# Kernel tuning notes

Measured on AMD Instinct MI355X. Metric: run time of the kernel, lower is better.

Reference implementation:

```python
import jax, jax.numpy as jnp
import numpy as np

N_LAYERS = 2
D_MODEL = 1024
D_INNER = 2 * D_MODEL
D_STATE = 16
D_CONV = 4
DT_RANK = D_MODEL // 16  # 64
B_SZ, L = 1, 2048
EPS = 1e-5


def layernorm(x, w, b):
    mu = jnp.mean(x, axis=-1, keepdims=True)
    var = jnp.mean(jnp.square(x - mu), axis=-1, keepdims=True)
    return (x - mu) * jax.lax.rsqrt(var + EPS) * w + b


def mamba(x, in_w, cw, cb, xp_w, dtp_w, dtp_b, A_log, Dp, out_w):
    # x: [B, L, D_MODEL]
    Bn, Ln, _ = x.shape
    xz = jnp.einsum('bld,ed->ble', x, in_w)          # [B,L,2*D_INNER]
    xc, z = jnp.split(xz, 2, axis=-1)
    # causal depthwise conv1d (kernel D_CONV)
    xp = jnp.pad(xc, ((0, 0), (D_CONV - 1, 0), (0, 0)))
    xc = sum(xp[:, k:k + Ln, :] * cw[:, k] for k in range(D_CONV)) + cb
    xc = jax.nn.silu(xc)
    dbl = jnp.einsum('ble,re->blr', xc, xp_w)        # [B,L,DT_RANK+2*D_STATE]
    dt, Bm, Cm = jnp.split(dbl, [DT_RANK, DT_RANK + D_STATE], axis=-1)
    dt = jax.nn.softplus(jnp.einsum('blr,er->ble', dt, dtp_w) + dtp_b)  # [B,L,E]
    A = -jnp.exp(A_log)                              # [E,N], strictly negative
    dA = jnp.exp(dt[..., None] * A)                  # [B,L,E,N]
    dBu = (dt * xc)[..., None] * Bm[:, :, None, :]   # [B,L,E,N]

    def step(h, inp):
        dA_t, dBu_t, C_t = inp
        h = dA_t * h + dBu_t                         # [B,E,N]
        y = jnp.einsum('ben,bn->be', h, C_t)
        return h, y

    h0 = jnp.zeros((Bn, D_INNER, D_STATE), dA.dtype)
    _, ys = jax.lax.scan(step, h0, (dA.transpose(1, 0, 2, 3),
                                    dBu.transpose(1, 0, 2, 3),
                                    Cm.transpose(1, 0, 2)))
    y = ys.transpose(1, 0, 2) + xc * Dp              # [B,L,E]
    y = y * jax.nn.silu(z)
    return jnp.einsum('ble,de->bld', y, out_w)       # [B,L,D_MODEL]


def setup_inputs() -> dict:
    key = jax.random.key(0)
    ks = jax.random.split(key, 12)
    s = 0.02
    dt_init = np.log(np.expm1(0.01)).astype(np.float32)  # softplus^-1(0.01)
    A_row = jnp.log(jnp.arange(1, D_STATE + 1, dtype=jnp.float32))
    return {
        'x': jax.random.normal(ks[0], (B_SZ, L, D_MODEL), jnp.float32),
        'ln_w': jnp.ones((N_LAYERS, D_MODEL), jnp.float32),
        'ln_b': jnp.zeros((N_LAYERS, D_MODEL), jnp.float32),
        'in_proj_w': jax.random.normal(ks[1], (N_LAYERS, 2 * D_INNER, D_MODEL)) * s,
        'conv_w': jax.random.normal(ks[2], (N_LAYERS, D_INNER, D_CONV)) * 0.2,
        'conv_b': jnp.zeros((N_LAYERS, D_INNER), jnp.float32),
        'x_proj_w': jax.random.normal(ks[3], (N_LAYERS, DT_RANK + 2 * D_STATE, D_INNER)) * s,
        'dt_proj_w': jax.random.normal(ks[4], (N_LAYERS, D_INNER, DT_RANK)) * (DT_RANK ** -0.5),
        'dt_proj_b': jnp.full((N_LAYERS, D_INNER), dt_init),
        'A_log': jnp.broadcast_to(A_row, (N_LAYERS, D_INNER, D_STATE)).copy(),
        'D_skip': jnp.ones((N_LAYERS, D_INNER), jnp.float32),
        'out_proj_w': jax.random.normal(ks[5], (N_LAYERS, D_MODEL, D_INNER)) * s,
        'norm_f_w': jnp.ones((D_MODEL,), jnp.float32),
        'norm_f_b': jnp.zeros((D_MODEL,), jnp.float32),
    }


def reference(x, ln_w, ln_b, in_proj_w, conv_w, conv_b, x_proj_w, dt_proj_w,
              dt_proj_b, A_log, D_skip, out_proj_w, norm_f_w, norm_f_b):
    for i in range(N_LAYERS):
        h = layernorm(x, ln_w[i], ln_b[i])
        h = mamba(h, in_proj_w[i], conv_w[i], conv_b[i], x_proj_w[i],
                  dt_proj_w[i], dt_proj_b[i], A_log[i], D_skip[i], out_proj_w[i])
        x = h + x  # residual (dropout/drop_path are identity in eval)
    return layernorm(x, norm_f_w, norm_f_b)
```

## Files before the change

### kernel.cpp

```cpp
#include <hip/hip_runtime.h>
#include <hip/hip_bf16.h>
#include <math.h>

#define LSEQ 2048
#define DMODEL 1024
#define DINNER 2048
#define DSTATE 16
#define DCONV 4
#define DTRANK 64
#define RPROJ 96

#define CHUNK 16
#define NCHUNK (LSEQ / CHUNK)

#define XSPLIT 4

typedef __attribute__((ext_vector_type(8))) short bf16x8;
typedef __attribute__((ext_vector_type(4))) float f32x4;

__device__ __forceinline__ float softplusf(float x) {
    return (x > 20.f) ? x : log1pf(__expf(x));
}
__device__ __forceinline__ float siluf(float x) {
    return x / (1.f + __expf(-x));
}
__device__ __forceinline__ short f2bf(float f) {
    union { float f; unsigned u; } v; v.f = f;
    unsigned r = v.u + 0x7FFFu + ((v.u >> 16) & 1u);
    return (short)(r >> 16);
}
__device__ __forceinline__ float bf2f(short h) {
    union { unsigned u; float f; } v;
    v.u = ((unsigned)(unsigned short)h) << 16;
    return v.f;
}

__device__ __forceinline__ void cvt8(const float* __restrict__ s,
                                     short* __restrict__ d, int i) {
    const float4 a = *(const float4*)(s + i);
    const float4 b = *(const float4*)(s + i + 4);
    alignas(16) short h[8];
    h[0] = f2bf(a.x); h[1] = f2bf(a.y); h[2] = f2bf(a.z); h[3] = f2bf(a.w);
    h[4] = f2bf(b.x); h[5] = f2bf(b.y); h[6] = f2bf(b.z); h[7] = f2bf(b.w);
    *(uint4*)(d + i) = *(const uint4*)h;
}

__global__ __launch_bounds__(256) void cvt_weights(
    const float* __restrict__ s0, short* __restrict__ d0, int n0,
    const float* __restrict__ s1, short* __restrict__ d1, int n1,
    const float* __restrict__ s2, short* __restrict__ d2, int n2,
    const float* __restrict__ s3, short* __restrict__ d3, int n3)
{
    int i = (blockIdx.x * 256 + threadIdx.x) * 8;
    if (i < n0) { cvt8(s0, d0, i); return; }
    i -= n0;
    if (i < n1) { cvt8(s1, d1, i); return; }
    i -= n1;
    if (i < n2) { cvt8(s2, d2, i); return; }
    i -= n2;
    if (i < n3) { cvt8(s3, d3, i); return; }
}

__global__ __launch_bounds__(256) void ln_kernel(
    const float* __restrict__ x, const float* __restrict__ w,
    const float* __restrict__ b, float* __restrict__ outf,
    short* __restrict__ outb)
{
    __shared__ float s1[256], s2[256];
    const int row = blockIdx.x;
    const int tid = threadIdx.x;
    const float* xr = x + (size_t)row * DMODEL;
    float v[4];
    float s = 0.f, sq = 0.f;
#pragma unroll
    for (int k = 0; k < 4; k++) {
        v[k] = xr[k * 256 + tid];
        s += v[k];
        sq += v[k] * v[k];
    }
    s1[tid] = s; s2[tid] = sq;
    __syncthreads();
    for (int off = 128; off > 0; off >>= 1) {
        if (tid < off) { s1[tid] += s1[tid + off]; s2[tid] += s2[tid + off]; }
        __syncthreads();
    }
    const float mu = s1[0] * (1.f / DMODEL);
    const float var = s2[0] * (1.f / DMODEL) - mu * mu;
    const float rstd = rsqrtf(var + 1e-5f);
#pragma unroll
    for (int k = 0; k < 4; k++) {
        const int i = k * 256 + tid;
        const float o = (v[k] - mu) * rstd * w[i] + b[i];
        if (outf) outf[(size_t)row * DMODEL + i] = o;
        if (outb) outb[(size_t)row * DMODEL + i] = f2bf(o);
    }
}

template<int MI, int NJ, int MODE>
__global__ __launch_bounds__(256) void gemm_mfma(
    const short* __restrict__ A, int lda,
    const short* __restrict__ W, int ldw,
    float* __restrict__ Cf, short* __restrict__ Cb, int ldc,
    int M, int N, int K,
    const float* __restrict__ resid)
{
    constexpr int BM = 32 * MI;
    constexpr int BN = 32 * NJ;
    constexpr int AISS = BM / 32;
    constexpr int WISS = BN / 32;
    __shared__ alignas(16) short As[BM * 64];
    __shared__ alignas(16) short Ws[BN * 64];

    const int tid = threadIdx.x;
    const int lane = tid & 63;
    const int w = tid >> 6;
    const int wr = w >> 1, wc = w & 1;
    const int row0 = blockIdx.y * BM;
    const int col0 = blockIdx.x * BN;
    const int kbeg = blockIdx.z * K;

    const int srow = tid >> 3;
    const int dch  = tid & 7;
    const int skch = (dch ^ (srow & 7)) * 8;

    f32x4 acc[MI][NJ];
#pragma unroll
    for (int i = 0; i < MI; i++)
#pragma unroll
        for (int j = 0; j < NJ; j++) acc[i][j] = (f32x4)0.f;

    const int lrow = lane & 15;
    const int q = lane >> 4;

    for (int kt = kbeg; kt < kbeg + K; kt += 64) {
        __syncthreads();
#pragma unroll
        for (int j = 0; j < AISS; j++) {
            const short* gp = A + (size_t)(row0 + j * 32 + srow) * lda + kt + skch;
            __builtin_amdgcn_global_load_lds(
                (const __attribute__((address_space(1))) void*)gp,
                (__attribute__((address_space(3))) void*)(&As[j * 2048 + tid * 8]),
                16, 0, 0);
        }
#pragma unroll
        for (int j = 0; j < WISS; j++) {
            const int wrow = col0 + j * 32 + srow;
            if (wrow < N) {
                const short* gp = W + (size_t)wrow * ldw + kt + skch;
                __builtin_amdgcn_global_load_lds(
                    (const __attribute__((address_space(1))) void*)gp,
                    (__attribute__((address_space(3))) void*)(&Ws[j * 2048 + tid * 8]),
                    16, 0, 0);
            }
        }
        __syncthreads();

#pragma unroll
        for (int ks = 0; ks < 2; ks++) {
            bf16x8 af[MI], bfr[NJ];
#pragma unroll
            for (int i = 0; i < MI; i++) {
                const int R = wr * (16 * MI) + i * 16 + lrow;
                const int pc = (ks * 4 + q) ^ (R & 7);
                af[i] = *(const bf16x8*)&As[R * 64 + pc * 8];
            }
#pragma unroll
            for (int j = 0; j < NJ; j++) {
                const int R = wc * (16 * NJ) + j * 16 + lrow;
                const int pc = (ks * 4 + q) ^ (R & 7);
                bfr[j] = *(const bf16x8*)&Ws[R * 64 + pc * 8];
            }
#pragma unroll
            for (int i = 0; i < MI; i++)
#pragma unroll
                for (int j = 0; j < NJ; j++)
                    acc[i][j] = __builtin_amdgcn_mfma_f32_16x16x32_bf16(
                        af[i], bfr[j], acc[i][j], 0, 0, 0);
        }
    }

    const int rbase = row0 + wr * (16 * MI);
    const int cbase = col0 + wc * (16 * NJ);
#pragma unroll
    for (int i = 0; i < MI; i++) {
#pragma unroll
        for (int j = 0; j < NJ; j++) {
            const int gcol = cbase + j * 16 + lrow;
            if (gcol < N) {
#pragma unroll
                for (int r = 0; r < 4; r++) {
                    const int grow = rbase + i * 16 + (lane >> 4) * 4 + r;
                    float v = acc[i][j][r];
                    if (MODE == 2) {
                        Cf[(size_t)grow * ldc + gcol] =
                            v + resid[(size_t)grow * ldc + gcol];
                    } else if (MODE == 3) {
                        Cb[(size_t)grow * ldc + gcol] = f2bf(v);
                    } else {
                        atomicAdd(&Cf[(size_t)grow * ldc + gcol], v);
                    }
                }
            }
        }
    }
}

__global__ __launch_bounds__(256) void dtproj_kernel(
    const float* __restrict__ dbl,
    const short* __restrict__ dtp_w,
    const float* __restrict__ dtp_b,
    short* __restrict__ dt_bf)
{
    __shared__ alignas(16) short As[64 * 32];
    __shared__ alignas(16) short Ws[128 * 32];
    const int tid = threadIdx.x;
    const int lane = tid & 63;
    const int w = tid >> 6;
    const int wr = w >> 1, wc = w & 1;
    const int row0 = blockIdx.y * 64;
    const int col0 = blockIdx.x * 128;
    const int srow = tid >> 2;
    const int skch = ((tid & 3) ^ ((srow >> 1) & 3)) * 8;
    const int lrow = lane & 15;
    const int q = lane >> 4;

    f32x4 acc[2][4];
#pragma unroll
    for (int i = 0; i < 2; i++)
#pragma unroll
        for (int j = 0; j < 4; j++) acc[i][j] = (f32x4)0.f;

#pragma unroll
    for (int kt = 0; kt < 64; kt += 32) {
        __syncthreads();
        {
            const float* gp = dbl + (size_t)(row0 + srow) * RPROJ + kt + skch;
            const float4 a = *(const float4*)gp;
            const float4 b = *(const float4*)(gp + 4);
            alignas(16) short h[8];
            h[0] = f2bf(a.x); h[1] = f2bf(a.y); h[2] = f2bf(a.z); h[3] = f2bf(a.w);
            h[4] = f2bf(b.x); h[5] = f2bf(b.y); h[6] = f2bf(b.z); h[7] = f2bf(b.w);
            *(uint4*)(As + tid * 8) = *(const uint4*)h;
        }
#pragma unroll
        for (int j = 0; j < 2; j++) {
            const short* gp = dtp_w + (size_t)(col0 + j * 64 + srow) * DTRANK + kt + skch;
            __builtin_amdgcn_global_load_lds(
                (const __attribute__((address_space(1))) void*)gp,
                (__attribute__((address_space(3))) void*)(&Ws[j * 2048 + tid * 8]),
                16, 0, 0);
        }
        __syncthreads();

        bf16x8 af[2], bfr[4];
#pragma unroll
        for (int i = 0; i < 2; i++) {
            const int R = wr * 32 + i * 16 + lrow;
            af[i] = *(const bf16x8*)&As[R * 32 + ((q ^ ((R >> 1) & 3)) * 8)];
        }
#pragma unroll
        for (int j = 0; j < 4; j++) {
            const int R = wc * 64 + j * 16 + lrow;
            bfr[j] = *(const bf16x8*)&Ws[R * 32 + ((q ^ ((R >> 1) & 3)) * 8)];
        }
#pragma unroll
        for (int i = 0; i < 2; i++)
#pragma unroll
            for (int j = 0; j < 4; j++)
                acc[i][j] = __builtin_amdgcn_mfma_f32_16x16x32_bf16(
                    af[i], bfr[j], acc[i][j], 0, 0, 0);
    }

    const int rbase = row0 + wr * 32;
    const int cbase = col0 + wc * 64;
#pragma unroll
    for (int i = 0; i < 2; i++)
#pragma unroll
        for (int j = 0; j < 4; j++) {
            const int gcol = cbase + j * 16 + lrow;
#pragma unroll
            for (int r = 0; r < 4; r++) {
                const int grow = rbase + i * 16 + (lane >> 4) * 4 + r;
                dt_bf[(size_t)grow * DINNER + gcol] =
                    f2bf(softplusf(acc[i][j][r] + dtp_b[gcol]));
            }
        }
}

__global__ __launch_bounds__(256) void conv_silu_kernel(
    const short* __restrict__ xzb, const float* __restrict__ cw,
    const float* __restrict__ cb, short* __restrict__ xcb,
    float* __restrict__ dbl_zero)
{
    const int g = blockIdx.x * 256 + threadIdx.x;
    if (g < (LSEQ * RPROJ) / 4)
        *(float4*)(dbl_zero + g * 4) = make_float4(0.f, 0.f, 0.f, 0.f);
    const int t = g >> 8;
    const int c0 = (g & 255) * 8;
    float acc[8];
#pragma unroll
    for (int j = 0; j < 8; j++) acc[j] = cb[c0 + j];
#pragma unroll
    for (int k = 0; k < DCONV; k++) {
        const int tt = t - (DCONV - 1) + k;
        if (tt >= 0) {
            const bf16x8 v = *(const bf16x8*)(xzb + (size_t)tt * (2 * DINNER) + c0);
#pragma unroll
            for (int j = 0; j < 8; j++)
                acc[j] += bf2f(v[j]) * cw[(c0 + j) * DCONV + k];
        }
    }
    alignas(16) short h[8];
#pragma unroll
    for (int j = 0; j < 8; j++) h[j] = f2bf(siluf(acc[j]));
    *(uint4*)(xcb + (size_t)t * DINNER + c0) = *(const uint4*)h;
}

__global__ __launch_bounds__(256) void scan_pass1(
    const short* __restrict__ dtb,
    const short* __restrict__ xcb,
    const float* __restrict__ dbl,
    const float* __restrict__ A_log,
    float* __restrict__ S,
    float* __restrict__ sumdt)
{
    const int e = blockIdx.x * 256 + threadIdx.x;
    const int c = blockIdx.y;
    float a[DSTATE];
#pragma unroll
    for (int n = 0; n < DSTATE; n++) a[n] = -__expf(A_log[(size_t)e * DSTATE + n]);
    float h[DSTATE];
#pragma unroll
    for (int n = 0; n < DSTATE; n++) h[n] = 0.f;
    float sd = 0.f;

    __shared__ float sBC[CHUNK][32];
    for (int i = threadIdx.x; i < CHUNK * 32; i += 256) {
        const int tl = i >> 5, j = i & 31;
        sBC[tl][j] = dbl[(size_t)(c * CHUNK + tl) * RPROJ + DTRANK + j];
    }
    __syncthreads();

    const size_t rb = (size_t)c * CHUNK * DINNER + e;
    short dt_c = dtb[rb], xc_c = xcb[rb];
#pragma unroll
    for (int tl = 0; tl < CHUNK; tl++) {
        short dt_n = 0, xc_n = 0;
        if (tl + 1 < CHUNK) {
            dt_n = dtb[rb + (size_t)(tl + 1) * DINNER];
            xc_n = xcb[rb + (size_t)(tl + 1) * DINNER];
        }
        const float dtv = bf2f(dt_c);
        const float du = dtv * bf2f(xc_c);
        sd += dtv;
#pragma unroll
        for (int n = 0; n < DSTATE; n++) {
            const float dA = __expf(dtv * a[n]);
            h[n] = dA * h[n] + du * sBC[tl][n];
        }
        dt_c = dt_n; xc_c = xc_n;
    }
    sumdt[(size_t)c * DINNER + e] = sd;
#pragma unroll
    for (int n = 0; n < DSTATE; n++)
        S[((size_t)c * DSTATE + n) * DINNER + e] = h[n];
}

__global__ __launch_bounds__(256) void scan_pass2(
    const float* __restrict__ A_log,
    const float* __restrict__ sumdt,
    float* __restrict__ S)
{
    const int idx = blockIdx.x * 256 + threadIdx.x;
    const int e = idx & (DINNER - 1);
    const int n = idx >> 11;
    const float a = -__expf(A_log[(size_t)e * DSTATE + n]);
    const size_t base = (size_t)n * DINNER + e;
    const size_t cstr = (size_t)DSTATE * DINNER;
    float H = 0.f;
    for (int c = 0; c < NCHUNK; c += 4) {
        const float sc0 = S[base + (size_t)(c + 0) * cstr];
        const float sc1 = S[base + (size_t)(c + 1) * cstr];
        const float sc2 = S[base + (size_t)(c + 2) * cstr];
        const float sc3 = S[base + (size_t)(c + 3) * cstr];
        const float sd0 = sumdt[(size_t)(c + 0) * DINNER + e];
        const float sd1 = sumdt[(size_t)(c + 1) * DINNER + e];
        const float sd2 = sumdt[(size_t)(c + 2) * DINNER + e];
        const float sd3 = sumdt[(size_t)(c + 3) * DINNER + e];
        S[base + (size_t)(c + 0) * cstr] = H;
        H = __expf(a * sd0) * H + sc0;
        S[base + (size_t)(c + 1) * cstr] = H;
        H = __expf(a * sd1) * H + sc1;
        S[base + (size_t)(c + 2) * cstr] = H;
        H = __expf(a * sd2) * H + sc2;
        S[base + (size_t)(c + 3) * cstr] = H;
        H = __expf(a * sd3) * H + sc3;
    }
}

__global__ __launch_bounds__(256) void scan_pass3(
    const short* __restrict__ dtb,
    const short* __restrict__ xcb,
    const float* __restrict__ dbl,
    const short* __restrict__ xzb,
    const float* __restrict__ A_log,
    const float* __restrict__ Dp,
    const float* __restrict__ S,
    short* __restrict__ yb)
{
    const int e = blockIdx.x * 256 + threadIdx.x;
    const int c = blockIdx.y;
    float a[DSTATE];
#pragma unroll
    for (int n = 0; n < DSTATE; n++) a[n] = -__expf(A_log[(size_t)e * DSTATE + n]);
    float h[DSTATE];
#pragma unroll
    for (int n = 0; n < DSTATE; n++)
        h[n] = S[((size_t)c * DSTATE + n) * DINNER + e];
    const float dskip = Dp[e];

    __shared__ float sBC[CHUNK][32];
    for (int i = threadIdx.x; i < CHUNK * 32; i += 256) {
        const int tl = i >> 5, j = i & 31;
        sBC[tl][j] = dbl[(size_t)(c * CHUNK + tl) * RPROJ + DTRANK + j];
    }
    __syncthreads();

    const size_t rb = (size_t)c * CHUNK * DINNER + e;
    const size_t zb = (size_t)c * CHUNK * (2 * DINNER) + DINNER + e;
    short dt_c = dtb[rb], xc_c = xcb[rb], z_c = xzb[zb];
#pragma unroll
    for (int tl = 0; tl < CHUNK; tl++) {
        short dt_n = 0, xc_n = 0, z_n = 0;
        if (tl + 1 < CHUNK) {
            dt_n = dtb[rb + (size_t)(tl + 1) * DINNER];
            xc_n = xcb[rb + (size_t)(tl + 1) * DINNER];
            z_n = xzb[zb + (size_t)(tl + 1) * (2 * DINNER)];
        }
        const float dtv = bf2f(dt_c);
        const float xcv = bf2f(xc_c);
        const float du = dtv * xcv;
        float yv = 0.f;
#pragma unroll
        for (int n = 0; n < DSTATE; n++) {
            const float dA = __expf(dtv * a[n]);
            h[n] = dA * h[n] + du * sBC[tl][n];
            yv += h[n] * sBC[tl][16 + n];
        }
        yv = (yv + xcv * dskip) * siluf(bf2f(z_c));
        yb[rb + (size_t)tl * DINNER] = f2bf(yv);
        dt_c = dt_n; xc_c = xc_n; z_c = z_n;
    }
}

extern "C" void kernel_launch(void* const* d_in, const int* in_sizes, int n_in,
                              void* d_out, int out_size, void* d_ws, size_t ws_size,
                              hipStream_t stream) {
    const float* x_in   = (const float*)d_in[0];
    const float* ln_w   = (const float*)d_in[1];
    const float* ln_b   = (const float*)d_in[2];
    const float* in_w   = (const float*)d_in[3];
    const float* conv_w = (const float*)d_in[4];
    const float* conv_b = (const float*)d_in[5];
    const float* xp_w   = (const float*)d_in[6];
    const float* dtp_w  = (const float*)d_in[7];
    const float* dtp_b  = (const float*)d_in[8];
    const float* A_log  = (const float*)d_in[9];
    const float* D_skip = (const float*)d_in[10];
    const float* out_w  = (const float*)d_in[11];
    const float* nf_w   = (const float*)d_in[12];
    const float* nf_b   = (const float*)d_in[13];
    float* out = (float*)d_out;

    float* w = (float*)d_ws;
    float* buf_x = w; w += (size_t)LSEQ * DMODEL;
    float* dbl   = w; w += (size_t)LSEQ * RPROJ;
    float* Sbuf  = w; w += (size_t)NCHUNK * DSTATE * DINNER;
    float* sumdt = w; w += (size_t)NCHUNK * DINNER;
    short* h_bf    = (short*)w; w += (size_t)LSEQ * DMODEL / 2;
    short* xz_bf   = (short*)w; w += (size_t)LSEQ * 2 * DINNER / 2;
    short* xc_bf   = (short*)w; w += (size_t)LSEQ * DINNER / 2;
    short* dt_bf   = (short*)w; w += (size_t)LSEQ * DINNER / 2;
    short* y_bf    = (short*)w; w += (size_t)LSEQ * DINNER / 2;
    short* in_w_bf  = (short*)w; w += (size_t)2 * (2 * DINNER) * DMODEL / 2;
    short* xp_w_bf  = (short*)w; w += (size_t)2 * RPROJ * DINNER / 2;
    short* dtp_w_bf = (short*)w; w += (size_t)2 * DINNER * DTRANK / 2;
    short* out_w_bf = (short*)w; w += (size_t)2 * DMODEL * DINNER / 2;

    {
        const int n1 = 2 * (2 * DINNER) * DMODEL;
        const int n2 = 2 * RPROJ * DINNER;
        const int n3 = 2 * DMODEL * DINNER;
        const int n4 = 2 * DINNER * DTRANK;
        const int total = n1 + n2 + n3 + n4;
        cvt_weights<<<dim3(total / (256 * 8)), dim3(256), 0, stream>>>(
            in_w, in_w_bf, n1, xp_w, xp_w_bf, n2,
            out_w, out_w_bf, n3, dtp_w, dtp_w_bf, n4);
    }

    for (int layer = 0; layer < 2; layer++) {
        const float* resid_src = (layer == 0) ? x_in : buf_x;
        ln_kernel<<<dim3(LSEQ), dim3(256), 0, stream>>>(
            resid_src, ln_w + layer * DMODEL, ln_b + layer * DMODEL,
            nullptr, h_bf);
        gemm_mfma<4, 4, 3><<<dim3((2 * DINNER) / 128, LSEQ / 128), dim3(256), 0, stream>>>(
            h_bf, DMODEL, in_w_bf + (size_t)layer * 2 * DINNER * DMODEL, DMODEL,
            nullptr, xz_bf, 2 * DINNER, LSEQ, 2 * DINNER, DMODEL, nullptr);
        conv_silu_kernel<<<dim3((LSEQ * DINNER / 8) / 256), dim3(256), 0, stream>>>(
            xz_bf, conv_w + (size_t)layer * DINNER * DCONV, conv_b + layer * DINNER,
            xc_bf, dbl);
        gemm_mfma<2, 2, 6><<<dim3(2, LSEQ / 64, XSPLIT), dim3(256), 0, stream>>>(
            xc_bf, DINNER, xp_w_bf + (size_t)layer * RPROJ * DINNER, DINNER,
            dbl, nullptr, RPROJ, LSEQ, RPROJ, DINNER / XSPLIT, nullptr);
        dtproj_kernel<<<dim3(DINNER / 128, LSEQ / 64), dim3(256), 0, stream>>>(
            dbl, dtp_w_bf + (size_t)layer * DINNER * DTRANK,
            dtp_b + layer * DINNER, dt_bf);
        const float* Al = A_log + (size_t)layer * DINNER * DSTATE;
        scan_pass1<<<dim3(DINNER / 256, NCHUNK), dim3(256), 0, stream>>>(
            dt_bf, xc_bf, dbl, Al, Sbuf, sumdt);
        scan_pass2<<<dim3((DINNER * DSTATE) / 256), dim3(256), 0, stream>>>(
            Al, sumdt, Sbuf);
        scan_pass3<<<dim3(DINNER / 256, NCHUNK), dim3(256), 0, stream>>>(
            dt_bf, xc_bf, dbl, xz_bf, Al, D_skip + layer * DINNER, Sbuf, y_bf);
        gemm_mfma<4, 2, 2><<<dim3(DMODEL / 64, LSEQ / 128), dim3(256), 0, stream>>>(
            y_bf, DINNER, out_w_bf + (size_t)layer * DMODEL * DINNER, DINNER,
            buf_x, nullptr, DMODEL, LSEQ, DMODEL, DINNER, resid_src);
    }
    ln_kernel<<<dim3(LSEQ), dim3(256), 0, stream>>>(buf_x, nf_w, nf_b, out, nullptr);
}
```

Measured before the change: 456.9 us.

## Fuse weight conversion with first layernorm, use wave-per-row LN, larger scan chunks

Merges the weight fp32-to-bf16 conversion kernel with the first layer's layernorm into one launch. Rewrites layernorm so each 64-lane wave handles one row with shuffle reductions instead of shared-memory tree reductions. Doubles the scan chunk size to halve the number of chunks carried between passes, and limits scan loop unrolling. This cuts launches and sync overhead, but longer chunks reduce scan parallelism.

```diff
diff --git a/kernel.cpp b/kernel.cpp
--- a/kernel.cpp
+++ b/kernel.cpp
@@ -10,7 +10,7 @@
 #define DTRANK 64
 #define RPROJ 96
 
-#define CHUNK 16
+#define CHUNK 32
 #define NCHUNK (LSEQ / CHUNK)
 
 #define XSPLIT 4
@@ -45,64 +45,81 @@
     *(uint4*)(d + i) = *(const uint4*)h;
 }
 
-__global__ __launch_bounds__(256) void cvt_weights(
-    const float* __restrict__ s0, short* __restrict__ d0, int n0,
-    const float* __restrict__ s1, short* __restrict__ d1, int n1,
-    const float* __restrict__ s2, short* __restrict__ d2, int n2,
-    const float* __restrict__ s3, short* __restrict__ d3, int n3)
-{
-    int i = (blockIdx.x * 256 + threadIdx.x) * 8;
-    if (i < n0) { cvt8(s0, d0, i); return; }
-    i -= n0;
-    if (i < n1) { cvt8(s1, d1, i); return; }
-    i -= n1;
-    if (i < n2) { cvt8(s2, d2, i); return; }
-    i -= n2;
-    if (i < n3) { cvt8(s3, d3, i); return; }
-}
-
-__global__ __launch_bounds__(256) void ln_kernel(
+__device__ __forceinline__ void ln_phase(
+    const float* __restrict__ x, const float* __restrict__ w,
+    const float* __restrict__ b, float* __restrict__ outf,
+    short* __restrict__ outb, int bid, int tid)
+{
+    const int wv = tid >> 6, lane = tid & 63;
+    const int row = bid * 4 + wv;
+    const float* xr = x + (size_t)row * DMODEL;
+    float v[16];
+    float s = 0.f, sq = 0.f;
+#pragma unroll
+    for (int k = 0; k < 16; k++) {
+        v[k] = xr[k * 64 + lane];
+        s += v[k];
+        sq += v[k] * v[k];
+    }
+#pragma unroll
+    for (int off = 32; off > 0; off >>= 1) {
+        s += __shfl_xor(s, off, 64);
+        sq += __shfl_xor(sq, off, 64);
+    }
+    const float mu = s * (1.f / DMODEL);
+    const float var = sq * (1.f / DMODEL) - mu * mu;
+    const float rstd = rsqrtf(var + 1e-5f);
+#pragma unroll
+    for (int k = 0; k < 16; k++) {
+        const int i = k * 64 + lane;
+        const float o = (v[k] - mu) * rstd * w[i] + b[i];
+        if (outf) outf[(size_t)row * DMODEL + i] = o;
+        else      outb[(size_t)row * DMODEL + i] = f2bf(o);
+    }
+}
+
+__global__ __launch_bounds__(256) void cvt_ln_kernel(
+    const float* __restrict__ in_w, short* __restrict__ in_w_bf,
+    const float* __restrict__ xp_w, short* __restrict__ xp_w_bf,
+    const float* __restrict__ out_w, short* __restrict__ out_w_bf,
+    const float* __restrict__ dtp_w, short* __restrict__ dtp_w_bf,
+    const float* __restrict__ x_in, const float* __restrict__ ln_w,
+    const float* __restrict__ ln_b, short* __restrict__ h_bf)
+{
+    const int n1 = 2 * (2 * DINNER) * DMODEL;
+    const int n2 = 2 * RPROJ * DINNER;
+    const int n3 = 2 * DMODEL * DINNER;
+    const int bid = blockIdx.x;
+    const int tid = threadIdx.x;
+    {
+        int i = (bid * 256 + tid) * 8;
+        if (i < n1) { cvt8(in_w, in_w_bf, i); goto done_cvt; }
+        i -= n1;
+        if (i < n2) { cvt8(xp_w, xp_w_bf, i); goto done_cvt; }
+        i -= n2;
+        if (i < n3) { cvt8(out_w, out_w_bf, i); goto done_cvt; }
+        i -= n3;
+        cvt8(dtp_w, dtp_w_bf, i);
+    }
+done_cvt:
+    if (bid < LSEQ / 4)
+        ln_phase(x_in, ln_w, ln_b, nullptr, h_bf, bid, tid);
+}
+
+__global__ __launch_bounds__(256) void ln_g(
     const float* __restrict__ x, const float* __restrict__ w,
     const float* __restrict__ b, float* __restrict__ outf,
     short* __restrict__ outb)
 {
-    __shared__ float s1[256], s2[256];
-    const int row = blockIdx.x;
-    const int tid = threadIdx.x;
-    const float* xr = x + (size_t)row * DMODEL;
-    float v[4];
-    float s = 0.f, sq = 0.f;
-#pragma unroll
-    for (int k = 0; k < 4; k++) {
-        v[k] = xr[k * 256 + tid];
-        s += v[k];
-        sq += v[k] * v[k];
-    }
-    s1[tid] = s; s2[tid] = sq;
-    __syncthreads();
-    for (int off = 128; off > 0; off >>= 1) {
-        if (tid < off) { s1[tid] += s1[tid + off]; s2[tid] += s2[tid + off]; }
-        __syncthreads();
-    }
-    const float mu = s1[0] * (1.f / DMODEL);
-    const float var = s2[0] * (1.f / DMODEL) - mu * mu;
-    const float rstd = rsqrtf(var + 1e-5f);
-#pragma unroll
-    for (int k = 0; k < 4; k++) {
-        const int i = k * 256 + tid;
-        const float o = (v[k] - mu) * rstd * w[i] + b[i];
-        if (outf) outf[(size_t)row * DMODEL + i] = o;
-        if (outb) outb[(size_t)row * DMODEL + i] = f2bf(o);
-    }
+    ln_phase(x, w, b, outf, outb, blockIdx.x, threadIdx.x);
 }
 
 template<int MI, int NJ, int MODE>
-__global__ __launch_bounds__(256) void gemm_mfma(
+__global__ __launch_bounds__(256) void gemm_g(
     const short* __restrict__ A, int lda,
     const short* __restrict__ W, int ldw,
     float* __restrict__ Cf, short* __restrict__ Cb, int ldc,
-    int M, int N, int K,
-    const float* __restrict__ resid)
+    int N, int K, const float* __restrict__ resid)
 {
     constexpr int BM = 32 * MI;
     constexpr int BN = 32 * NJ;
@@ -205,7 +222,7 @@
     }
 }
 
-__global__ __launch_bounds__(256) void dtproj_kernel(
+__global__ __launch_bounds__(256) void dtproj_g(
     const float* __restrict__ dbl,
     const short* __restrict__ dtp_w,
     const float* __restrict__ dtp_b,
@@ -287,7 +304,7 @@
         }
 }
 
-__global__ __launch_bounds__(256) void conv_silu_kernel(
+__global__ __launch_bounds__(256) void conv_g(
     const short* __restrict__ xzb, const float* __restrict__ cw,
     const float* __restrict__ cb, short* __restrict__ xcb,
     float* __restrict__ dbl_zero)
@@ -316,7 +333,7 @@
     *(uint4*)(xcb + (size_t)t * DINNER + c0) = *(const uint4*)h;
 }
 
-__global__ __launch_bounds__(256) void scan_pass1(
+__global__ __launch_bounds__(256) void scan1_g(
     const short* __restrict__ dtb,
     const short* __restrict__ xcb,
     const float* __restrict__ dbl,
@@ -343,7 +360,7 @@
 
     const size_t rb = (size_t)c * CHUNK * DINNER + e;
     short dt_c = dtb[rb], xc_c = xcb[rb];
-#pragma unroll
+#pragma unroll 4
     for (int tl = 0; tl < CHUNK; tl++) {
         short dt_n = 0, xc_n = 0;
         if (tl + 1 < CHUNK) {
@@ -366,7 +383,7 @@
         S[((size_t)c * DSTATE + n) * DINNER + e] = h[n];
 }
 
-__global__ __launch_bounds__(256) void scan_pass2(
+__global__ __launch_bounds__(256) void scan2_g(
     const float* __restrict__ A_log,
     const float* __restrict__ sumdt,
     float* __restrict__ S)
@@ -398,7 +415,7 @@
     }
 }
 
-__global__ __launch_bounds__(256) void scan_pass3(
+__global__ __launch_bounds__(256) void scan3_g(
     const short* __restrict__ dtb,
     const short* __restrict__ xcb,
     const float* __restrict__ dbl,
@@ -429,7 +446,7 @@
     const size_t rb = (size_t)c * CHUNK * DINNER + e;
     const size_t zb = (size_t)c * CHUNK * (2 * DINNER) + DINNER + e;
     short dt_c = dtb[rb], xc_c = xcb[rb], z_c = xzb[zb];
-#pragma unroll
+#pragma unroll 4
     for (int tl = 0; tl < CHUNK; tl++) {
         short dt_n = 0, xc_n = 0, z_n = 0;
         if (tl + 1 < CHUNK) {
@@ -488,43 +505,41 @@
     short* out_w_bf = (short*)w; w += (size_t)2 * DMODEL * DINNER / 2;
 
     {
-        const int n1 = 2 * (2 * DINNER) * DMODEL;
-        const int n2 = 2 * RPROJ * DINNER;
-        const int n3 = 2 * DMODEL * DINNER;
-        const int n4 = 2 * DINNER * DTRANK;
-        const int total = n1 + n2 + n3 + n4;
-        cvt_weights<<<dim3(total / (256 * 8)), dim3(256), 0, stream>>>(
-            in_w, in_w_bf, n1, xp_w, xp_w_bf, n2,
-            out_w, out_w_bf, n3, dtp_w, dtp_w_bf, n4);
+        const int total = 2 * (2 * DINNER) * DMODEL + 2 * RPROJ * DINNER
+                        + 2 * DMODEL * DINNER + 2 * DINNER * DTRANK;
+        cvt_ln_kernel<<<dim3(total / (256 * 8)), dim3(256), 0, stream>>>(
+            in_w, in_w_bf, xp_w, xp_w_bf, out_w, out_w_bf, dtp_w, dtp_w_bf,
+            x_in, ln_w, ln_b, h_bf);
     }
 
     for (int layer = 0; layer < 2; layer++) {
         const float* resid_src = (layer == 0) ? x_in : buf_x;
-        ln_kernel<<<dim3(LSEQ), dim3(256), 0, stream>>>(
-            resid_src, ln_w + layer * DMODEL, ln_b + layer * DMODEL,
-            nullptr, h_bf);
-        gemm_mfma<4, 4, 3><<<dim3((2 * DINNER) / 128, LSEQ / 128), dim3(256), 0, stream>>>(
+        if (layer > 0)
+            ln_g<<<dim3(LSEQ / 4), dim3(256), 0, stream>>>(
+                resid_src, ln_w + layer * DMODEL, ln_b + layer * DMODEL,
+                nullptr, h_bf);
+        gemm_g<4, 4, 3><<<dim3((2 * DINNER) / 128, LSEQ / 128), dim3(256), 0, stream>>>(
             h_bf, DMODEL, in_w_bf + (size_t)layer * 2 * DINNER * DMODEL, DMODEL,
-            nullptr, xz_bf, 2 * DINNER, LSEQ, 2 * DINNER, DMODEL, nullptr);
-        conv_silu_kernel<<<dim3((LSEQ * DINNER / 8) / 256), dim3(256), 0, stream>>>(
+            nullptr, xz_bf, 2 * DINNER, 2 * DINNER, DMODEL, nullptr);
+        conv_g<<<dim3((LSEQ * DINNER / 8) / 256), dim3(256), 0, stream>>>(
             xz_bf, conv_w + (size_t)layer * DINNER * DCONV, conv_b + layer * DINNER,
             xc_bf, dbl);
-        gemm_mfma<2, 2, 6><<<dim3(2, LSEQ / 64, XSPLIT), dim3(256), 0, stream>>>(
+        gemm_g<2, 2, 6><<<dim3(2, LSEQ / 64, XSPLIT), dim3(256), 0, stream>>>(
             xc_bf, DINNER, xp_w_bf + (size_t)layer * RPROJ * DINNER, DINNER,
-            dbl, nullptr, RPROJ, LSEQ, RPROJ, DINNER / XSPLIT, nullptr);
-        dtproj_kernel<<<dim3(DINNER / 128, LSEQ / 64), dim3(256), 0, stream>>>(
+            dbl, nullptr, RPROJ, RPROJ, DINNER / XSPLIT, nullptr);
+        dtproj_g<<<dim3(DINNER / 128, LSEQ / 64), dim3(256), 0, stream>>>(
             dbl, dtp_w_bf + (size_t)layer * DINNER * DTRANK,
             dtp_b + layer * DINNER, dt_bf);
         const float* Al = A_log + (size_t)layer * DINNER * DSTATE;
-        scan_pass1<<<dim3(DINNER / 256, NCHUNK), dim3(256), 0, stream>>>(
+        scan1_g<<<dim3(DINNER / 256, NCHUNK), dim3(256), 0, stream>>>(
             dt_bf, xc_bf, dbl, Al, Sbuf, sumdt);
-        scan_pass2<<<dim3((DINNER * DSTATE) / 256), dim3(256), 0, stream>>>(
+        scan2_g<<<dim3((DINNER * DSTATE) / 256), dim3(256), 0, stream>>>(
             Al, sumdt, Sbuf);
-        scan_pass3<<<dim3(DINNER / 256, NCHUNK), dim3(256), 0, stream>>>(
+        scan3_g<<<dim3(DINNER / 256, NCHUNK), dim3(256), 0, stream>>>(
             dt_bf, xc_bf, dbl, xz_bf, Al, D_skip + layer * DINNER, Sbuf, y_bf);
-        gemm_mfma<4, 2, 2><<<dim3(DMODEL / 64, LSEQ / 128), dim3(256), 0, stream>>>(
+        gemm_g<4, 2, 2><<<dim3(DMODEL / 64, LSEQ / 128), dim3(256), 0, stream>>>(
             y_bf, DINNER, out_w_bf + (size_t)layer * DMODEL * DINNER, DINNER,
-            buf_x, nullptr, DMODEL, LSEQ, DMODEL, DINNER, resid_src);
-    }
-    ln_kernel<<<dim3(LSEQ), dim3(256), 0, stream>>>(buf_x, nf_w, nf_b, out, nullptr);
-}
+            buf_x, nullptr, DMODEL, DMODEL, DINNER, resid_src);
+    }
+    ln_g<<<dim3(LSEQ / 4), dim3(256), 0, stream>>>(buf_x, nf_w, nf_b, out, nullptr);
+}
```

Result: slower. 476.1 us (+4.2%).
